# Kernel optimization log

Measured on AMD Instinct MI355X. Metric: run time of the kernel, lower is better.

Reference implementation:

```python
import jax, jax.numpy as jnp
import numpy as np

N = 524288      # total trajectory tokens
D_MODEL = 256
HIDDEN = 512
OUT_DIM = 32
N_TYPES = 4


def setup_inputs() -> dict:
    key = jax.random.key(0)
    k1, k2, k3, k4 = jax.random.split(key, 4)
    x = jax.random.normal(k1, (N, D_MODEL), dtype=jnp.float32)
    types = jax.random.randint(k2, (N,), 0, N_TYPES, dtype=jnp.int64)
    W1 = jax.random.normal(k3, (N_TYPES, D_MODEL, HIDDEN), dtype=jnp.float32) / np.sqrt(D_MODEL)
    b1 = jnp.zeros((N_TYPES, HIDDEN), dtype=jnp.float32)
    W2 = jax.random.normal(k4, (N_TYPES, HIDDEN, OUT_DIM), dtype=jnp.float32) / np.sqrt(HIDDEN)
    b2 = jnp.zeros((N_TYPES, OUT_DIM), dtype=jnp.float32)
    return {"x": x, "types": types, "W1": W1, "b1": b1, "W2": W2, "b2": b2}


def reference(x, types, W1, b1, W2, b2):
    # Type-masked gather -> per-type MLP decode -> scatter back to original order.
    # The gather/argsort-scatter of the torch code is equivalent (for equal
    # per-type output dims) to computing each type's decoder and selecting the
    # rows where types == type_id; we loop over the small fixed set of types.
    n_types = W1.shape[0]
    out = jnp.zeros((x.shape[0], W2.shape[-1]), dtype=x.dtype)
    for t in range(n_types):
        h = jax.nn.relu(x @ W1[t] + b1[t])          # [N, HIDDEN]
        y = h @ W2[t] + b2[t]                        # [N, OUT_DIM]
        out = jnp.where((types == t)[:, None], y, out)
    return out
```

## Files before the change

### kernel.cpp

```cpp
#include <hip/hip_runtime.h>
#include <hip/hip_bf16.h>
#include <hip/hip_fp16.h>

#define N_TOK 524288
#define DM 256
#define HID 512
#define OUTD 32
#define NTYPE 4
#define BM 256
#define MT 4
#define HC 32
#define NCHUNK (HID / HC)
#define CHUNK_BYTES (HC * DM * 2)
#define NBLK 512
#define GX1D (N_TOK / BM + NTYPE)
#define HS_STRIDE 80

typedef _Float16 half8 __attribute__((ext_vector_type(8)));
typedef float f32x4 __attribute__((ext_vector_type(4)));


__global__ void count_kernel(const int* __restrict__ types, int* __restrict__ bc) {
    __shared__ int c[NTYPE];
    int tid = threadIdx.x;
    if (tid < NTYPE) c[tid] = 0;
    __syncthreads();
    int b = blockIdx.x;
    int lane = tid & 63;
    #pragma unroll
    for (int j = 0; j < 4; ++j) {
        int t = types[b * 1024 + j * 256 + tid];
        #pragma unroll
        for (int tt = 0; tt < NTYPE; ++tt) {
            unsigned long long mask = __ballot(t == tt);
            if (lane == 0) atomicAdd(&c[tt], __popcll(mask));
        }
    }
    __syncthreads();
    if (tid < NTYPE) bc[tid * NBLK + b] = c[tid];
}

__global__ void scan_blocks_kernel(const int* __restrict__ bc,
                                   int* __restrict__ bb,
                                   int* __restrict__ meta) {
    __shared__ int totals[NTYPE];
    __shared__ int typeoff[NTYPE];
    int wave = threadIdx.x >> 6, lane = threadIdx.x & 63;
    int excl[NBLK / 64];
    int running = 0;
    #pragma unroll
    for (int it = 0; it < NBLK / 64; ++it) {
        int v = bc[wave * NBLK + it * 64 + lane];
        int s = v;
        #pragma unroll
        for (int d = 1; d < 64; d <<= 1) {
            int u = __shfl_up(s, d);
            if (lane >= d) s += u;
        }
        excl[it] = running + s - v;
        running += __shfl(s, 63);
    }
    if (lane == 0) totals[wave] = running;
    __syncthreads();
    if (threadIdx.x == 0) {
        int off = 0, toff = 0;
        for (int tt = 0; tt < NTYPE; ++tt) {
            typeoff[tt] = off;
            meta[tt] = totals[tt];
            meta[4 + tt] = off;
            meta[8 + tt] = toff;
            off += totals[tt];
            toff += (totals[tt] + BM - 1) / BM;
        }
        meta[12] = toff;
    }
    __syncthreads();
    #pragma unroll
    for (int it = 0; it < NBLK / 64; ++it)
        bb[wave * NBLK + it * 64 + lane] = typeoff[wave] + excl[it];
}

__global__ void scatter2_kernel(const int* __restrict__ types,
                                const int* __restrict__ bb,
                                int* __restrict__ idx) {
    __shared__ int base[NTYPE];
    __shared__ int wcnt[4][NTYPE];
    int b = blockIdx.x;
    int tid = threadIdx.x, wave = tid >> 6, lane = tid & 63;
    if (tid < NTYPE) base[tid] = bb[tid * NBLK + b];
    #pragma unroll
    for (int j = 0; j < 4; ++j) {
        __syncthreads();
        int i = b * 1024 + j * 256 + tid;
        int t = types[i];
        int rank = 0;
        #pragma unroll
        for (int tt = 0; tt < NTYPE; ++tt) {
            unsigned long long mask = __ballot(t == tt);
            if (t == tt) rank = __popcll(mask & ((1ull << lane) - 1ull));
            if (lane == 0) wcnt[wave][tt] = __popcll(mask);
        }
        __syncthreads();
        int pre = 0;
        for (int w = 0; w < wave; ++w) pre += wcnt[w][t];
        idx[base[t] + pre + rank] = i;
        __syncthreads();
        if (tid < NTYPE) {
            int tot = 0;
            #pragma unroll
            for (int w = 0; w < 4; ++w) tot += wcnt[w][tid];
            base[tid] += tot;
        }
    }
}


__global__ void wprep_kernel(const float* __restrict__ W1, const float* __restrict__ W2,
                             _Float16* __restrict__ W1T, _Float16* __restrict__ W2T) {
    int i = blockIdx.x * blockDim.x + threadIdx.x;
    if (i < NTYPE * HID * DM) {
        int t = i / (HID * DM);
        int r = i - t * (HID * DM);
        int byteoff = r * 2;
        int hc = byteoff / CHUNK_BYTES;
        int rem = byteoff - hc * CHUNK_BYTES;
        int hr = rem >> 9;
        int brow = rem & 511;
        int d = (brow ^ ((hr & 7) << 4)) >> 1;
        int h = hc * HC + hr;
        W1T[i] = (_Float16)W1[(t * DM + d) * HID + h];
    }
    if (i < NTYPE * OUTD * HID) {
        int t = i / (OUTD * HID);
        int r = i - t * (OUTD * HID);
        int o = r / HID;
        int h = r - o * HID;
        W2T[i] = (_Float16)W2[(t * HID + h) * OUTD + o];
    }
}


__launch_bounds__(256, 2)
__global__ void fused_mlp_kernel(const float* __restrict__ x,
                                 const int* __restrict__ meta,
                                 const int* __restrict__ idx,
                                 const _Float16* __restrict__ W1T,
                                 const _Float16* __restrict__ W2T,
                                 const float* __restrict__ b1,
                                 const float* __restrict__ b2,
                                 float* __restrict__ out) {
    const int b = blockIdx.x;
    if (b >= meta[12]) return;
    const int t = (b >= meta[9]) + (b >= meta[10]) + (b >= meta[11]);
    const int cnt = meta[t];
    const int row_base = (b - meta[8 + t]) * BM;
    const int* idx_t = idx + meta[4 + t];

    __shared__ __align__(16) char W1sB[2][CHUNK_BYTES];
    __shared__ __align__(16) char HsB[4][64 * HS_STRIDE];
    __shared__ float b1s[HID];

    const int tid = threadIdx.x;
    const int wave = tid >> 6;
    const int lane = tid & 63;
    const int l15 = lane & 15;
    const int lg = lane >> 4;

    {
        float2 bv = *(const float2*)(b1 + t * HID + tid * 2);
        b1s[tid * 2] = bv.x;
        b1s[tid * 2 + 1] = bv.y;
    }

    half8 afrag[MT][8];
    #pragma unroll
    for (int mt = 0; mt < MT; ++mt) {
        int rl = wave * 64 + mt * 16 + l15;
        int rglob = idx_t[min(row_base + rl, cnt - 1)];
        const float* xr = x + (size_t)rglob * DM;
        #pragma unroll
        for (int kk = 0; kk < 8; ++kk) {
            int k0 = kk * 32 + lg * 8;
            f32x4 v0 = __builtin_nontemporal_load((const f32x4*)(xr + k0));
            f32x4 v1 = __builtin_nontemporal_load((const f32x4*)(xr + k0 + 4));
            half8 h;
            h[0] = (_Float16)v0[0]; h[1] = (_Float16)v0[1];
            h[2] = (_Float16)v0[2]; h[3] = (_Float16)v0[3];
            h[4] = (_Float16)v1[0]; h[5] = (_Float16)v1[1];
            h[6] = (_Float16)v1[2]; h[7] = (_Float16)v1[3];
            afrag[mt][kk] = h;
        }
    }

    const f32x4 fzero = {0.f, 0.f, 0.f, 0.f};
    f32x4 acc2[MT][2];
    #pragma unroll
    for (int mt = 0; mt < MT; ++mt)
        #pragma unroll
        for (int nt = 0; nt < 2; ++nt)
            acc2[mt][nt] = fzero;

    const char* w1base = (const char*)(W1T + (size_t)t * HID * DM);
    const _Float16* w2t_t = W2T + (size_t)t * OUTD * HID;
    char* myHs = HsB[wave];

    #pragma unroll
    for (int it = 0; it < 4; ++it) {
        __builtin_amdgcn_global_load_lds(
            (const __attribute__((address_space(1))) void*)(w1base + it * 4096 + tid * 16),
            (__attribute__((address_space(3))) void*)(&W1sB[0][it * 4096 + tid * 16]),
            16, 0, 0);
    }
    half8 w2A[2], w2B[2];
    #pragma unroll
    for (int nt = 0; nt < 2; ++nt)
        w2A[nt] = *(const half8*)(w2t_t + (nt * 16 + l15) * HID + lg * 8);
    __syncthreads();

#define CHUNK_BODY(HCI, W2USE, W2FILL)                                          \
    {                                                                           \
        const int hc = (HCI);                                                   \
        const char* cur = W1sB[hc & 1];                                         \
        if (hc + 1 < NCHUNK) {                                                  \
            const char* src = w1base + (size_t)(hc + 1) * CHUNK_BYTES;          \
            char* dst = W1sB[(hc + 1) & 1];                                     \
            _Pragma("unroll")                                                   \
            for (int it = 0; it < 4; ++it) {                                    \
                __builtin_amdgcn_global_load_lds(                               \
                    (const __attribute__((address_space(1))) void*)(src + it * 4096 + tid * 16), \
                    (__attribute__((address_space(3))) void*)(dst + it * 4096 + tid * 16),       \
                    16, 0, 0);                                                  \
            }                                                                   \
        }                                                                       \
        {                 \
            int hn = (hc + 1) & 15;                                             \
            _Pragma("unroll")                                                   \
            for (int nt = 0; nt < 2; ++nt)                                      \
                W2FILL[nt] = *(const half8*)(w2t_t + (nt * 16 + l15) * HID + hn * HC + lg * 8); \
        }                                                                       \
        f32x4 acc1[MT][2];                                                      \
        _Pragma("unroll")                                                       \
        for (int mt = 0; mt < MT; ++mt)                                         \
            _Pragma("unroll")                                                   \
            for (int nt = 0; nt < 2; ++nt)                                      \
                acc1[mt][nt] = fzero;                                           \
        _Pragma("unroll")                                                       \
        for (int kk = 0; kk < 8; ++kk) {                                        \
            half8 bfr[2];                                                       \
            _Pragma("unroll")                                                   \
            for (int nt = 0; nt < 2; ++nt) {                                    \
                int hr = nt * 16 + l15;                                         \
                bfr[nt] = *(const half8*)(cur + hr * 512 +                      \
                            ((kk * 64 + lg * 16) ^ ((hr & 7) << 4)));           \
            }                                                                   \
            _Pragma("unroll")                                                   \
            for (int mt = 0; mt < MT; ++mt)                                     \
                _Pragma("unroll")                                               \
                for (int nt = 0; nt < 2; ++nt)                                  \
                    acc1[mt][nt] = __builtin_amdgcn_mfma_f32_16x16x32_f16(      \
                        afrag[mt][kk], bfr[nt], acc1[mt][nt], 0, 0, 0);         \
        }                                                                       \
            \
        _Pragma("unroll")                                                       \
        for (int nt = 0; nt < 2; ++nt) {                                        \
            int col = nt * 16 + l15;                                            \
            float bias = b1s[hc * HC + col];                                    \
            _Pragma("unroll")                                                   \
            for (int mt = 0; mt < MT; ++mt) {                                   \
                _Pragma("unroll")                                               \
                for (int j = 0; j < 4; ++j) {                                   \
                    float v = fmaxf(acc1[mt][nt][j] + bias, 0.f);               \
                    int rl = mt * 16 + lg * 4 + j;                              \
                    *(_Float16*)(myHs + rl * HS_STRIDE + col * 2) = (_Float16)v;\
                }                                                               \
            }                                                                   \
        }                                                                       \
                                          \
        half8 a2[MT];                                                           \
        _Pragma("unroll")                                                       \
        for (int mt = 0; mt < MT; ++mt) {                                       \
            int rl = mt * 16 + l15;                                             \
            a2[mt] = *(const half8*)(myHs + rl * HS_STRIDE + lg * 16);          \
        }                                                                       \
        _Pragma("unroll")                                                       \
        for (int mt = 0; mt < MT; ++mt)                                         \
            _Pragma("unroll")                                                   \
            for (int nt = 0; nt < 2; ++nt)                                      \
                acc2[mt][nt] = __builtin_amdgcn_mfma_f32_16x16x32_f16(          \
                    a2[mt], W2USE[nt], acc2[mt][nt], 0, 0, 0);                  \
        __syncthreads();   \
    }

    #pragma unroll
    for (int h2 = 0; h2 < NCHUNK; h2 += 2) {
        CHUNK_BODY(h2, w2A, w2B);
        CHUNK_BODY(h2 + 1, w2B, w2A);
    }
#undef CHUNK_BODY

    const int m = min(BM, cnt - row_base);
    #pragma unroll
    for (int mt = 0; mt < MT; ++mt) {
        #pragma unroll
        for (int j = 0; j < 4; ++j) {
            int rloc = wave * 64 + mt * 16 + lg * 4 + j;
            if (rloc < m) {
                int gr = idx_t[row_base + rloc];
                #pragma unroll
                for (int nt = 0; nt < 2; ++nt) {
                    int col = nt * 16 + l15;
                    float v = acc2[mt][nt][j] + b2[t * OUTD + col];
                    __builtin_nontemporal_store(v, &out[(size_t)gr * OUTD + col]);
                }
            }
        }
    }
}


extern "C" void kernel_launch(void* const* d_in, const int* in_sizes, int n_in,
                              void* d_out, int out_size, void* d_ws, size_t ws_size,
                              hipStream_t stream) {
    const float* x   = (const float*)d_in[0];
    const int* types = (const int*)d_in[1];
    const float* W1  = (const float*)d_in[2];
    const float* b1  = (const float*)d_in[3];
    const float* W2  = (const float*)d_in[4];
    const float* b2  = (const float*)d_in[5];
    float* out = (float*)d_out;

    char* ws = (char*)d_ws;
    int* meta = (int*)ws;
    int* idx = (int*)(ws + 64);
    _Float16* W1T = (_Float16*)(ws + 64 + 4 * (size_t)N_TOK);
    _Float16* W2T = W1T + (size_t)NTYPE * HID * DM;
    int* bc = (int*)W1T;
    int* bb = bc + NTYPE * NBLK;

    count_kernel<<<NBLK, 256, 0, stream>>>(types, bc);
    scan_blocks_kernel<<<1, 256, 0, stream>>>(bc, bb, meta);
    scatter2_kernel<<<NBLK, 256, 0, stream>>>(types, bb, idx);
    wprep_kernel<<<(NTYPE * HID * DM) / 256, 256, 0, stream>>>(W1, W2, W1T, W2T);

    fused_mlp_kernel<<<GX1D, 256, 0, stream>>>(x, meta, idx, W1T, W2T, b1, b2, out);
}
```

Measured before the change: 280.1 us.

## Keep hidden activations in registers by transposing MFMA operands, drop LDS staging

Swaps the A/B operands of the first-layer MFMA so each lane holds a transposed accumulator fragment. That fragment can be converted directly into the B-operand layout of the second-layer MFMA, with W2T pre-permuted to match. This removes the per-chunk LDS write/read round trip of the hidden activations and the associated LDS footprint. The output epilogue also becomes vectorized float4 stores per row, since the transposed accumulator holds contiguous columns.

```diff
diff --git a/kernel.cpp b/kernel.cpp
--- a/kernel.cpp
+++ b/kernel.cpp
@@ -14,7 +14,6 @@
 #define CHUNK_BYTES (HC * DM * 2)
 #define NBLK 512
 #define GX1D (N_TOK / BM + NTYPE)
-#define HS_STRIDE 80
 
 typedef _Float16 half8 __attribute__((ext_vector_type(8)));
 typedef float f32x4 __attribute__((ext_vector_type(4)));
@@ -134,7 +133,12 @@
         int t = i / (OUTD * HID);
         int r = i - t * (OUTD * HID);
         int o = r / HID;
-        int h = r - o * HID;
+        int pg = r - o * HID;
+        int hc = pg >> 5;
+        int p = pg & 31;
+        int lg = p >> 3, j = p & 7;
+        int h1 = (j < 4) ? (lg * 4 + j) : (16 + lg * 4 + (j - 4));
+        int h = hc * HC + h1;
         W2T[i] = (_Float16)W2[(t * HID + h) * OUTD + o];
     }
 }
@@ -157,8 +161,7 @@
     const int* idx_t = idx + meta[4 + t];
 
     __shared__ __align__(16) char W1sB[2][CHUNK_BYTES];
-    __shared__ __align__(16) char HsB[4][64 * HS_STRIDE];
-    __shared__ float b1s[HID];
+    __shared__ __align__(16) float b1s[HID];
 
     const int tid = threadIdx.x;
     const int wave = tid >> 6;
@@ -202,7 +205,6 @@
 
     const char* w1base = (const char*)(W1T + (size_t)t * HID * DM);
     const _Float16* w2t_t = W2T + (size_t)t * OUTD * HID;
-    char* myHs = HsB[wave];
 
     #pragma unroll
     for (int it = 0; it < 4; ++it) {
@@ -238,7 +240,7 @@
             for (int nt = 0; nt < 2; ++nt)                                      \
                 W2FILL[nt] = *(const half8*)(w2t_t + (nt * 16 + l15) * HID + hn * HC + lg * 8); \
         }                                                                       \
-        f32x4 acc1[MT][2];                                                      \
+        f32x4 acc1[MT][2];    \
         _Pragma("unroll")                                                       \
         for (int mt = 0; mt < MT; ++mt)                                         \
             _Pragma("unroll")                                                   \
@@ -258,36 +260,26 @@
                 _Pragma("unroll")                                               \
                 for (int nt = 0; nt < 2; ++nt)                                  \
                     acc1[mt][nt] = __builtin_amdgcn_mfma_f32_16x16x32_f16(      \
-                        afrag[mt][kk], bfr[nt], acc1[mt][nt], 0, 0, 0);         \
+                        bfr[nt], afrag[mt][kk], acc1[mt][nt], 0, 0, 0);         \
         }                                                                       \
-            \
-        _Pragma("unroll")                                                       \
-        for (int nt = 0; nt < 2; ++nt) {                                        \
-            int col = nt * 16 + l15;                                            \
-            float bias = b1s[hc * HC + col];                                    \
+              \
+        {                                                                       \
+            f32x4 bv0 = *(const f32x4*)(b1s + hc * HC + lg * 4);                \
+            f32x4 bv1 = *(const f32x4*)(b1s + hc * HC + 16 + lg * 4);           \
             _Pragma("unroll")                                                   \
             for (int mt = 0; mt < MT; ++mt) {                                   \
+                half8 hfrag;                                                    \
                 _Pragma("unroll")                                               \
                 for (int j = 0; j < 4; ++j) {                                   \
-                    float v = fmaxf(acc1[mt][nt][j] + bias, 0.f);               \
-                    int rl = mt * 16 + lg * 4 + j;                              \
-                    *(_Float16*)(myHs + rl * HS_STRIDE + col * 2) = (_Float16)v;\
+                    hfrag[j]     = (_Float16)fmaxf(acc1[mt][0][j] + bv0[j], 0.f);\
+                    hfrag[4 + j] = (_Float16)fmaxf(acc1[mt][1][j] + bv1[j], 0.f);\
                 }                                                               \
+                _Pragma("unroll")                                               \
+                for (int nt = 0; nt < 2; ++nt)                                  \
+                    acc2[mt][nt] = __builtin_amdgcn_mfma_f32_16x16x32_f16(      \
+                        W2USE[nt], hfrag, acc2[mt][nt], 0, 0, 0);               \
             }                                                                   \
         }                                                                       \
-                                          \
-        half8 a2[MT];                                                           \
-        _Pragma("unroll")                                                       \
-        for (int mt = 0; mt < MT; ++mt) {                                       \
-            int rl = mt * 16 + l15;                                             \
-            a2[mt] = *(const half8*)(myHs + rl * HS_STRIDE + lg * 16);          \
-        }                                                                       \
-        _Pragma("unroll")                                                       \
-        for (int mt = 0; mt < MT; ++mt)                                         \
-            _Pragma("unroll")                                                   \
-            for (int nt = 0; nt < 2; ++nt)                                      \
-                acc2[mt][nt] = __builtin_amdgcn_mfma_f32_16x16x32_f16(          \
-                    a2[mt], W2USE[nt], acc2[mt][nt], 0, 0, 0);                  \
         __syncthreads();   \
     }
 
@@ -299,19 +291,19 @@
 #undef CHUNK_BODY
 
     const int m = min(BM, cnt - row_base);
+    f32x4 b2v[2];
+    #pragma unroll
+    for (int nt = 0; nt < 2; ++nt)
+        b2v[nt] = *(const f32x4*)(b2 + t * OUTD + nt * 16 + lg * 4);
     #pragma unroll
     for (int mt = 0; mt < MT; ++mt) {
-        #pragma unroll
-        for (int j = 0; j < 4; ++j) {
-            int rloc = wave * 64 + mt * 16 + lg * 4 + j;
-            if (rloc < m) {
-                int gr = idx_t[row_base + rloc];
-                #pragma unroll
-                for (int nt = 0; nt < 2; ++nt) {
-                    int col = nt * 16 + l15;
-                    float v = acc2[mt][nt][j] + b2[t * OUTD + col];
-                    __builtin_nontemporal_store(v, &out[(size_t)gr * OUTD + col]);
-                }
+        int rloc = wave * 64 + mt * 16 + l15;
+        if (rloc < m) {
+            int gr = idx_t[row_base + rloc];
+            #pragma unroll
+            for (int nt = 0; nt < 2; ++nt) {
+                f32x4 v = acc2[mt][nt] + b2v[nt];
+                __builtin_nontemporal_store(v, (f32x4*)(out + (size_t)gr * OUTD + nt * 16 + lg * 4));
             }
         }
     }
```

Measured after the change: 266.4 us. -4.9%, faster.
